# Kernel tuning notes

Hardware: AMD Instinct MI355X
Metric: run time of the kernel (lower is better)

## Reference

```python
import jax, jax.numpy as jnp
import numpy as np
from jax import lax

TRAJ_STEPS = 50  # output_dim=100 -> 50 (x,y) waypoints


def setup_inputs() -> dict:
    key = jax.random.key(0)
    ks = jax.random.split(key, 12)
    s = 0.05  # small init scale to keep gates out of saturation
    return {
        "x": jax.random.normal(ks[0], (32768, 256), jnp.float32),
        "W1": jax.random.normal(ks[1], (256, 64), jnp.float32) * s,
        "b1": jax.random.normal(ks[2], (64,), jnp.float32) * s,
        "W2": jax.random.normal(ks[3], (64, 64), jnp.float32) * s,
        "b2": jax.random.normal(ks[4], (64,), jnp.float32) * s,
        "Wih": jax.random.normal(ks[5], (2, 192), jnp.float32) * s,   # GRU input weights, gate order (r,z,n)
        "bih": jax.random.normal(ks[6], (192,), jnp.float32) * s,
        "Whh": jax.random.normal(ks[7], (64, 192), jnp.float32) * s,  # GRU hidden weights
        "bhh": jax.random.normal(ks[8], (192,), jnp.float32) * s,
        "Wout": jax.random.normal(ks[9], (64, 2), jnp.float32) * s,
        "bout": jax.random.normal(ks[10], (2,), jnp.float32) * s,
    }


def _forward(x, W1, b1, W2, b2, Wih, bih, Whh, bhh, Wout, bout):
    H = W2.shape[1]
    # backbone MLP -> initial hidden state
    z = jax.nn.relu(x @ W1 + b1)
    z = jax.nn.relu(z @ W2 + b2)  # [B, H]

    def step(carry, _):
        wp, h = carry                      # wp: [B,2] current waypoint, h: [B,H]
        gi = wp @ Wih + bih                # [B, 3H]
        gh = h @ Whh + bhh                 # [B, 3H]
        ir, iz, inn = gi[..., :H], gi[..., H:2 * H], gi[..., 2 * H:]
        hr, hz, hn = gh[..., :H], gh[..., H:2 * H], gh[..., 2 * H:]
        r = jax.nn.sigmoid(ir + hr)
        u = jax.nn.sigmoid(iz + hz)
        n = jnp.tanh(inn + r * hn)
        h_new = (1.0 - u) * n + u * h      # PyTorch GRUCell update
        dx = jax.nn.sigmoid(h_new @ Wout + bout)  # [B,2]
        wp_new = wp + dx                   # residual accumulation
        return (wp_new, h_new), wp_new

    wp0 = jnp.zeros(x.shape[:-1] + (2,), z.dtype)
    _, wps = lax.scan(step, (wp0, z), None, length=TRAJ_STEPS)  # [T, B, 2]
    wps = jnp.moveaxis(wps, 0, -2)                              # [B, T, 2]
    return wps.reshape(x.shape[:-1] + (2 * TRAJ_STEPS,))        # [B, 2T]


def reference(x, W1, b1, W2, b2, Wih, bih, Whh, bhh, Wout, bout):
    return _forward(x, W1, b1, W2, b2, Wih, bih, Whh, bhh, Wout, bout)
```

## Files before the change

kernel.cpp:

```cpp
#include <hip/hip_runtime.h>
#include <hip/hip_bf16.h>

#define TRAJ 50

typedef __attribute__((ext_vector_type(8))) short short8;
typedef __attribute__((ext_vector_type(4))) float f32x4;
typedef __attribute__((ext_vector_type(2))) float f32x2;

#if defined(__has_builtin)
#if __has_builtin(__builtin_amdgcn_exp2f)
#define EXP2F(x) __builtin_amdgcn_exp2f(x)
#else
#define EXP2F(x) exp2f(x)
#endif
#if __has_builtin(__builtin_amdgcn_rcpf)
#define RCPF(x) __builtin_amdgcn_rcpf(x)
#else
#define RCPF(x) (1.0f/(x))
#endif
#else
#define EXP2F(x) exp2f(x)
#define RCPF(x) (1.0f/(x))
#endif

#define BAR() asm volatile("s_waitcnt lgkmcnt(0)\n\ts_barrier" ::: "memory")

__device__ __forceinline__ unsigned short f2bf(float f){
  union { float f; unsigned u; } v; v.f = f;
  unsigned u = v.u;
  u += 0x7FFFu + ((u >> 16) & 1u);
  return (unsigned short)(u >> 16);
}
__device__ __forceinline__ unsigned pk(unsigned short a, unsigned short b){
  return (unsigned)a | ((unsigned)b << 16);
}
__device__ __forceinline__ unsigned pkbf(float a, float b){
  union { __hip_bfloat162 h; unsigned u; } c;
  c.h = __float22bfloat162_rn(make_float2(a, b));
  return c.u;
}

#define MFMA16(A,B,C) __builtin_amdgcn_mfma_f32_16x16x32_bf16((A),(B),(C),0,0,0)

#define SSC (-1.44269504f)
#define TSC ( 2.88539008f)

__device__ __forceinline__ f32x2 exp2v(f32x2 v){ return (f32x2){EXP2F(v[0]), EXP2F(v[1])}; }
__device__ __forceinline__ f32x2 rcpv (f32x2 v){ return (f32x2){RCPF(v[0]), RCPF(v[1])}; }

__device__ __forceinline__ f32x2 gru_pair(f32x2 r_, f32x2 u_, f32x2 n_, f32x2 i_, f32x2 hp){
  const f32x2 one = (f32x2){1.f, 1.f};
  f32x2 d1 = exp2v(r_) + one;
  f32x2 d2 = exp2v(u_) + one;
  f32x2 rp = rcpv(d1 * d2);
  f32x2 rv = d2 * rp;
  f32x2 uv = d1 * rp;
  f32x2 y  = __builtin_elementwise_fma(rv, n_, i_);
  f32x2 nv = one - 2.f * rcpv(exp2v(y) + one);
  return __builtin_elementwise_fma(uv, hp - nv, nv);
}

__device__ __forceinline__ short8 gatherA(const float* __restrict__ M, int N,
                                          int k0, int i, float scale){
  const float* qp = M + (size_t)k0 * N + i;
  union { unsigned u[4]; short8 s; } c;
  #pragma unroll
  for (int j = 0; j < 4; ++j){
    float a = qp[(2*j  ) * N];
    float b = qp[(2*j+1) * N];
    c.u[j] = pk(f2bf(scale * a), f2bf(scale * b));
  }
  return c.s;
}

__global__ __launch_bounds__(256, 4) void gru_actor_kernel(
    const float* __restrict__ x,
    const float* __restrict__ W1, const float* __restrict__ b1,
    const float* __restrict__ W2, const float* __restrict__ b2,
    const float* __restrict__ Wih, const float* __restrict__ bih,
    const float* __restrict__ Whh, const float* __restrict__ bhh,
    const float* __restrict__ Wout, const float* __restrict__ bout,
    float* __restrict__ out)
{
  __shared__ __align__(16) char sm_h[4096];

  const int t    = threadIdx.x;
  const int q    = t >> 6;
  const int l    = t & 63;
  const int lr   = l & 15;
  const int lg   = l >> 4;
  const int rowbase = blockIdx.x * 16;
  const int dimq = q * 16;
  const int swz  = (lr & 7) << 4;
  const int colw = 32 * q + 8 * lg;

  f32x4 acc1;
  { float4 bv = *(const float4*)(b1 + dimq + 4 * lg);
    acc1 = (f32x4){bv.x, bv.y, bv.z, bv.w}; }
  {
    const float* xrow = x + (size_t)(rowbase + lr) * 256;
    #pragma unroll
    for (int kb = 0; kb < 8; ++kb){
      int k0 = kb * 32 + lg * 8;
      float4 xa = *(const float4*)(xrow + k0);
      float4 xb = *(const float4*)(xrow + k0 + 4);
      union { unsigned u[4]; short8 s; } bc;
      bc.u[0] = pkbf(xa.x, xa.y); bc.u[1] = pkbf(xa.z, xa.w);
      bc.u[2] = pkbf(xb.x, xb.y); bc.u[3] = pkbf(xb.z, xb.w);
      short8 A = gatherA(W1, 64, k0, dimq + lr, 1.0f);
      acc1 = MFMA16(A, bc.s, acc1);
    }
  }
  *(uint2*)(sm_h + lr * 128 + (colw ^ swz)) =
      make_uint2(pkbf(fmaxf(acc1[0],0.f), fmaxf(acc1[1],0.f)),
                 pkbf(fmaxf(acc1[2],0.f), fmaxf(acc1[3],0.f)));
  __syncthreads();

  f32x2 h2[2];
  {
    f32x4 acc2;
    float4 bv = *(const float4*)(b2 + dimq + 4 * lg);
    acc2 = (f32x4){bv.x, bv.y, bv.z, bv.w};
    #pragma unroll
    for (int kb = 0; kb < 2; ++kb){
      short8 B = *(const short8*)(sm_h + lr * 128 + ((kb * 64 + 16 * lg) ^ swz));
      short8 A = gatherA(W2, 64, kb * 32 + lg * 8, dimq + lr, 1.0f);
      acc2 = MFMA16(A, B, acc2);
    }
    h2[0] = (f32x2){fmaxf(acc2[0],0.f), fmaxf(acc2[1],0.f)};
    h2[1] = (f32x2){fmaxf(acc2[2],0.f), fmaxf(acc2[3],0.f)};
    *(uint2*)(sm_h + 2048 + lr * 128 + (colw ^ swz)) =
        make_uint2(pkbf(h2[0][0], h2[0][1]), pkbf(h2[1][0], h2[1][1]));
  }

  short8 Ah[3][2];
  #pragma unroll
  for (int g = 0; g < 3; ++g){
    float sc = (g < 2) ? SSC : TSC;
    #pragma unroll
    for (int kb = 0; kb < 2; ++kb)
      Ah[g][kb] = gatherA(Whh, 192, kb * 32 + lg * 8, g * 64 + dimq + lr, sc);
  }
  short8 Ak2f[4];
  {
    union { unsigned u[4]; short8 s; } c;
    c.u[0] = c.u[1] = c.u[2] = c.u[3] = 0u;
    int dr = dimq + lr, du = 64 + dr, dn = 128 + dr;
    if (lg == 0){
      c.u[0] = pk(f2bf(SSC*Wih[dr]), f2bf(SSC*Wih[192+dr]));
      c.u[1] = pk(f2bf(SSC*(bih[dr]+bhh[dr])), 0);
    }
    Ak2f[0] = c.s;
    c.u[0] = c.u[1] = 0u;
    if (lg == 0){
      c.u[0] = pk(f2bf(SSC*Wih[du]), f2bf(SSC*Wih[192+du]));
      c.u[1] = pk(f2bf(SSC*(bih[du]+bhh[du])), 0);
    }
    Ak2f[1] = c.s;
    c.u[0] = c.u[1] = 0u;
    if (lg == 0){
      c.u[1] = pk(f2bf(TSC*bhh[dn]), 0);
    }
    Ak2f[2] = c.s;
    c.u[0] = c.u[1] = 0u;
    if (lg == 0){
      c.u[0] = pk(f2bf(TSC*Wih[dn]), f2bf(TSC*Wih[192+dn]));
      c.u[1] = pk(f2bf(TSC*bih[dn]), 0);
    }
    Ak2f[3] = c.s;
  }
  short8 AoR[2];
  #pragma unroll
  for (int kb = 0; kb < 2; ++kb){
    short8 f = (short8){0,0,0,0,0,0,0,0};
    if (lr < 2){
      #pragma unroll
      for (int j = 0; j < 8; ++j){
        int k = kb * 32 + lg * 8 + j;
        f[j] = (short)f2bf(SSC * Wout[k * 2 + lr]);
      }
    }
    AoR[kb] = f;
  }
  f32x4 aD0 = (f32x4){0,0,0,0};
  if (lg == 0){ aD0[0] = SSC * bout[0]; aD0[1] = SSC * bout[1]; }
  const unsigned b2hi = (lg == 0) ? 0x00003F80u : 0u;
  const bool dostore = (lg == 0 && q == 0);
  const int rd0 = lr * 128 + ((0  + 16 * lg) ^ swz);
  const int rd1 = lr * 128 + ((64 + 16 * lg) ^ swz);
  const int wr0 = lr * 128 + (colw ^ swz);
  __syncthreads();

  float wp0 = 0.f, wp1 = 0.f;
  float* outp = out + (size_t)(rowbase + lr) * 100;
  short8 B0 = *(const short8*)(sm_h + 2048 + rd0);
  short8 B1 = *(const short8*)(sm_h + 2048 + rd1);

  #pragma unroll 2
  for (int s = 0; s < TRAJ; ++s){
    char* bufW = sm_h + ((s & 1) << 11);
    short8 B2;
    {
      union { unsigned u[4]; short8 sv; } c;
      c.u[0] = (lg == 0) ? pkbf(wp0, wp1) : 0u;
      c.u[1] = b2hi; c.u[2] = 0u; c.u[3] = 0u;
      B2 = c.sv;
    }
    f32x4 aR = (f32x4){0,0,0,0}, aU = (f32x4){0,0,0,0};
    f32x4 aN = (f32x4){0,0,0,0}, aI = (f32x4){0,0,0,0};
    aR = MFMA16(Ah[0][0], B0, aR);
    aR = MFMA16(Ah[0][1], B1, aR);
    aR = MFMA16(Ak2f[0],  B2, aR);
    aU = MFMA16(Ah[1][0], B0, aU);
    aU = MFMA16(Ah[1][1], B1, aU);
    aU = MFMA16(Ak2f[1],  B2, aU);
    aN = MFMA16(Ah[2][0], B0, aN);
    aN = MFMA16(Ah[2][1], B1, aN);
    aN = MFMA16(Ak2f[2],  B2, aN);
    aI = MFMA16(Ak2f[3],  B2, aI);
    f32x2 hA = gru_pair((f32x2){aR[0],aR[1]}, (f32x2){aU[0],aU[1]},
                        (f32x2){aN[0],aN[1]}, (f32x2){aI[0],aI[1]}, h2[0]);
    f32x2 hB = gru_pair((f32x2){aR[2],aR[3]}, (f32x2){aU[2],aU[3]},
                        (f32x2){aN[2],aN[3]}, (f32x2){aI[2],aI[3]}, h2[1]);
    h2[0] = hA; h2[1] = hB;
    *(uint2*)(bufW + wr0) =
        make_uint2(pkbf(hA[0], hA[1]), pkbf(hB[0], hB[1]));
    BAR();
    short8 nB0 = *(const short8*)(bufW + rd0);
    short8 nB1 = *(const short8*)(bufW + rd1);
    f32x4 aD = aD0;
    aD = MFMA16(AoR[0], nB0, aD);
    aD = MFMA16(AoR[1], nB1, aD);
    {
      float ea = EXP2F(aD[0]), eb = EXP2F(aD[1]);
      float da = 1.f + ea, db = 1.f + eb;
      float rp = RCPF(da * db);
      wp0 += db * rp;
      wp1 += da * rp;
    }
    if (dostore)
      *(float2*)(outp + 2 * s) = make_float2(wp0, wp1);
    B0 = nB0; B1 = nB1;
  }
}

extern "C" void kernel_launch(void* const* d_in, const int* in_sizes, int n_in,
                              void* d_out, int out_size, void* d_ws, size_t ws_size,
                              hipStream_t stream) {
  (void)n_in; (void)out_size; (void)d_ws; (void)ws_size;
  const float* x    = (const float*)d_in[0];
  const float* W1   = (const float*)d_in[1];
  const float* b1   = (const float*)d_in[2];
  const float* W2   = (const float*)d_in[3];
  const float* b2   = (const float*)d_in[4];
  const float* Wih  = (const float*)d_in[5];
  const float* bih  = (const float*)d_in[6];
  const float* Whh  = (const float*)d_in[7];
  const float* bhh  = (const float*)d_in[8];
  const float* Wout = (const float*)d_in[9];
  const float* bout = (const float*)d_in[10];
  float* out = (float*)d_out;

  int nrows = in_sizes[0] / 256;
  int grid  = nrows / 16;
  gru_actor_kernel<<<dim3(grid), dim3(256), 0, stream>>>(
      x, W1, b1, W2, b2, Wih, bih, Whh, bhh, Wout, bout, out);
}
```

Before: 111.8 us.

## Move constant MFMA operand fragments to LDS to raise occupancy

Stores the augmented input/bias fragments and output-projection fragments in shared memory, reloading them every recurrence step instead of keeping them in registers. The launch bound is raised from 4 to 5 blocks per CU so the freed VGPRs can allow more resident waves. Lanes with zero fragments point at a zeroed LDS region, and asm barriers keep the compiler from hoisting the loads back out of the loop. The cost is six extra LDS reads per step and about 6KB more LDS per block.

```diff
diff --git a/kernel.cpp b/kernel.cpp
--- a/kernel.cpp
+++ b/kernel.cpp
@@ -73,7 +73,7 @@
   return c.s;
 }
 
-__global__ __launch_bounds__(256, 4) void gru_actor_kernel(
+__global__ __launch_bounds__(256, 5) void gru_actor_kernel(
     const float* __restrict__ x,
     const float* __restrict__ W1, const float* __restrict__ b1,
     const float* __restrict__ W2, const float* __restrict__ b2,
@@ -83,6 +83,7 @@
     float* __restrict__ out)
 {
   __shared__ __align__(16) char sm_h[4096];
+  __shared__ __align__(16) char sm_aug[1024 + 4 * 1280];
 
   const int t    = threadIdx.x;
   const int q    = t >> 6;
@@ -94,6 +95,8 @@
   const int swz  = (lr & 7) << 4;
   const int colw = 32 * q + 8 * lg;
 
+  *(unsigned*)(sm_aug + t * 4) = 0u;
+
   f32x4 acc1;
   { float4 bv = *(const float4*)(b1 + dimq + 4 * lg);
     acc1 = (f32x4){bv.x, bv.y, bv.z, bv.w}; }
@@ -141,47 +144,32 @@
     for (int kb = 0; kb < 2; ++kb)
       Ah[g][kb] = gatherA(Whh, 192, kb * 32 + lg * 8, g * 64 + dimq + lr, sc);
   }
-  short8 Ak2f[4];
-  {
-    union { unsigned u[4]; short8 s; } c;
-    c.u[0] = c.u[1] = c.u[2] = c.u[3] = 0u;
+  char* wq = sm_aug + 1024 + q * 1280;
+  if (lg == 0){
     int dr = dimq + lr, du = 64 + dr, dn = 128 + dr;
-    if (lg == 0){
-      c.u[0] = pk(f2bf(SSC*Wih[dr]), f2bf(SSC*Wih[192+dr]));
-      c.u[1] = pk(f2bf(SSC*(bih[dr]+bhh[dr])), 0);
-    }
-    Ak2f[0] = c.s;
-    c.u[0] = c.u[1] = 0u;
-    if (lg == 0){
-      c.u[0] = pk(f2bf(SSC*Wih[du]), f2bf(SSC*Wih[192+du]));
-      c.u[1] = pk(f2bf(SSC*(bih[du]+bhh[du])), 0);
-    }
-    Ak2f[1] = c.s;
-    c.u[0] = c.u[1] = 0u;
-    if (lg == 0){
-      c.u[1] = pk(f2bf(TSC*bhh[dn]), 0);
-    }
-    Ak2f[2] = c.s;
-    c.u[0] = c.u[1] = 0u;
-    if (lg == 0){
-      c.u[0] = pk(f2bf(TSC*Wih[dn]), f2bf(TSC*Wih[192+dn]));
-      c.u[1] = pk(f2bf(TSC*bih[dn]), 0);
-    }
-    Ak2f[3] = c.s;
-  }
-  short8 AoR[2];
-  #pragma unroll
-  for (int kb = 0; kb < 2; ++kb){
-    short8 f = (short8){0,0,0,0,0,0,0,0};
-    if (lr < 2){
+    *(uint4*)(wq +   0 + lr*16) = make_uint4(pk(f2bf(SSC*Wih[dr]), f2bf(SSC*Wih[192+dr])),
+                                             pk(f2bf(SSC*(bih[dr]+bhh[dr])), 0), 0u, 0u);
+    *(uint4*)(wq + 256 + lr*16) = make_uint4(pk(f2bf(SSC*Wih[du]), f2bf(SSC*Wih[192+du])),
+                                             pk(f2bf(SSC*(bih[du]+bhh[du])), 0), 0u, 0u);
+    *(uint4*)(wq + 512 + lr*16) = make_uint4(0u, pk(f2bf(TSC*bhh[dn]), 0), 0u, 0u);
+    *(uint4*)(wq + 768 + lr*16) = make_uint4(pk(f2bf(TSC*Wih[dn]), f2bf(TSC*Wih[192+dn])),
+                                             pk(f2bf(TSC*bih[dn]), 0), 0u, 0u);
+  }
+  if (lr < 2){
+    #pragma unroll
+    for (int kb = 0; kb < 2; ++kb){
+      unsigned w_[4];
       #pragma unroll
-      for (int j = 0; j < 8; ++j){
-        int k = kb * 32 + lg * 8 + j;
-        f[j] = (short)f2bf(SSC * Wout[k * 2 + lr]);
+      for (int j4 = 0; j4 < 4; ++j4){
+        int k = kb * 32 + lg * 8 + 2 * j4;
+        w_[j4] = pk(f2bf(SSC * Wout[k * 2 + lr]), f2bf(SSC * Wout[(k + 1) * 2 + lr]));
       }
-    }
-    AoR[kb] = f;
-  }
+      *(uint4*)(wq + 1024 + kb * 128 + (lr * 4 + lg) * 16) = make_uint4(w_[0], w_[1], w_[2], w_[3]);
+    }
+  }
+  unsigned off_ak = (lg == 0) ? (unsigned)(1024 + q * 1280 + lr * 16) : 0u;
+  unsigned off_ao = (lr <  2) ? (unsigned)(1024 + q * 1280 + 1024 + (lr * 4 + lg) * 16) : 0u;
+
   f32x4 aD0 = (f32x4){0,0,0,0};
   if (lg == 0){ aD0[0] = SSC * bout[0]; aD0[1] = SSC * bout[1]; }
   const unsigned b2hi = (lg == 0) ? 0x00003F80u : 0u;
@@ -206,18 +194,23 @@
       c.u[1] = b2hi; c.u[2] = 0u; c.u[3] = 0u;
       B2 = c.sv;
     }
+    asm volatile("" : "+v"(off_ak));
+    short8 AkR = *(const short8*)(sm_aug + off_ak);
+    short8 AkU = *(const short8*)(sm_aug + off_ak + 256);
+    short8 AkN = *(const short8*)(sm_aug + off_ak + 512);
+    short8 AkI = *(const short8*)(sm_aug + off_ak + 768);
     f32x4 aR = (f32x4){0,0,0,0}, aU = (f32x4){0,0,0,0};
     f32x4 aN = (f32x4){0,0,0,0}, aI = (f32x4){0,0,0,0};
     aR = MFMA16(Ah[0][0], B0, aR);
     aR = MFMA16(Ah[0][1], B1, aR);
-    aR = MFMA16(Ak2f[0],  B2, aR);
+    aR = MFMA16(AkR,      B2, aR);
     aU = MFMA16(Ah[1][0], B0, aU);
     aU = MFMA16(Ah[1][1], B1, aU);
-    aU = MFMA16(Ak2f[1],  B2, aU);
+    aU = MFMA16(AkU,      B2, aU);
     aN = MFMA16(Ah[2][0], B0, aN);
     aN = MFMA16(Ah[2][1], B1, aN);
-    aN = MFMA16(Ak2f[2],  B2, aN);
-    aI = MFMA16(Ak2f[3],  B2, aI);
+    aN = MFMA16(AkN,      B2, aN);
+    aI = MFMA16(AkI,      B2, aI);
     f32x2 hA = gru_pair((f32x2){aR[0],aR[1]}, (f32x2){aU[0],aU[1]},
                         (f32x2){aN[0],aN[1]}, (f32x2){aI[0],aI[1]}, h2[0]);
     f32x2 hB = gru_pair((f32x2){aR[2],aR[3]}, (f32x2){aU[2],aU[3]},
@@ -226,11 +219,14 @@
     *(uint2*)(bufW + wr0) =
         make_uint2(pkbf(hA[0], hA[1]), pkbf(hB[0], hB[1]));
     BAR();
+    asm volatile("" : "+v"(off_ao));
     short8 nB0 = *(const short8*)(bufW + rd0);
     short8 nB1 = *(const short8*)(bufW + rd1);
+    short8 Ao0 = *(const short8*)(sm_aug + off_ao);
+    short8 Ao1 = *(const short8*)(sm_aug + off_ao + 128);
     f32x4 aD = aD0;
-    aD = MFMA16(AoR[0], nB0, aD);
-    aD = MFMA16(AoR[1], nB1, aD);
+    aD = MFMA16(Ao0, nB0, aD);
+    aD = MFMA16(Ao1, nB1, aD);
     {
       float ea = EXP2F(aD[0]), eb = EXP2F(aD[1]);
       float da = 1.f + ea, db = 1.f + eb;
```

Result: slower. 114.7 us (+2.5%).
